# Kernel tuning notes

Measured on AMD Instinct MI355X. Metric: run time of the kernel, lower is better.

The kernel has to match this reference:

```python
import jax, jax.numpy as jnp
import numpy as np

HIDDEN = 1024
HEADS = 16
D_K = HIDDEN // HEADS
B, S = 2, 2048


def setup_inputs() -> dict:
    key = jax.random.key(0)
    ks = jax.random.split(key, 11)
    sc = 1.0 / np.sqrt(HIDDEN)
    return {
        "query": jax.random.normal(ks[0], (B, S, HIDDEN), jnp.float32),
        "key": jax.random.normal(ks[1], (B, S, HIDDEN), jnp.float32),
        "value": jax.random.normal(ks[2], (B, S, HIDDEN), jnp.float32),
        "w_q": jax.random.normal(ks[3], (HIDDEN, HIDDEN), jnp.float32) * sc,
        "b_q": jax.random.normal(ks[4], (HIDDEN,), jnp.float32) * 0.02,
        "w_k": jax.random.normal(ks[5], (HIDDEN, HIDDEN), jnp.float32) * sc,
        "b_k": jax.random.normal(ks[6], (HIDDEN,), jnp.float32) * 0.02,
        "w_v": jax.random.normal(ks[7], (HIDDEN, HIDDEN), jnp.float32) * sc,
        "b_v": jax.random.normal(ks[8], (HIDDEN,), jnp.float32) * 0.02,
        "w_o": jax.random.normal(ks[9], (HIDDEN, HIDDEN), jnp.float32) * sc,
        "b_o": jax.random.normal(ks[10], (HIDDEN,), jnp.float32) * 0.02,
    }


def reference(query, key, value, w_q, b_q, w_k, b_k, w_v, b_v, w_o, b_o):
    b, s, _ = query.shape
    # linear projections (torch Linear: x @ W^T + b)
    q = query @ w_q.T + b_q
    k = key @ w_k.T + b_k
    v = value @ w_v.T + b_v
    # [B, H, S, D]
    q = q.reshape(b, s, HEADS, D_K).transpose(0, 2, 1, 3)
    k = k.reshape(b, s, HEADS, D_K).transpose(0, 2, 1, 3)
    v = v.reshape(b, s, HEADS, D_K).transpose(0, 2, 1, 3)
    scale = jnp.float32(1.0 / np.sqrt(D_K))
    scores = jnp.einsum('bhqd,bhkd->bhqk', q, k) * scale  # [B,H,S,S]
    probs = jax.nn.softmax(scores, axis=-1)
    y = jnp.einsum('bhqk,bhkd->bhqd', probs, v)
    y = y.transpose(0, 2, 1, 3).reshape(b, s, HIDDEN)
    return y @ w_o.T + b_o
```

## Files before the change

### kernel.cpp

```cpp
#include <hip/hip_runtime.h>
#include <hip/hip_bf16.h>
#include <math.h>

#define HIDDEN 1024
#define HEADS 16
#define DK 64
#define BB 2
#define SS 2048
#define MROWS (BB*SS)

typedef __attribute__((ext_vector_type(8))) short short8;
typedef __attribute__((ext_vector_type(4))) float f32x4;
typedef __attribute__((ext_vector_type(16))) float f32x16;
typedef __attribute__((ext_vector_type(4))) unsigned short ushort4_t;

static __device__ __forceinline__ unsigned short f2bf(float f) {
    unsigned int u = __float_as_uint(f);
    u += 0x7fffu + ((u >> 16) & 1u);
    return (unsigned short)(u >> 16);
}
static __device__ __forceinline__ float bf2f(unsigned short s) {
    return __uint_as_float(((unsigned int)s) << 16);
}

static __device__ __forceinline__ unsigned int cvtpk(float lo, float hi) {
    unsigned int r;
    asm volatile("v_cvt_pk_bf16_f32 %0, %1, %2" : "=v"(r) : "v"(lo), "v"(hi));
    return r;
}
static __device__ __forceinline__ void swap32(unsigned int& a, unsigned int& b) {
    asm volatile("v_permlane32_swap_b32 %0, %1" : "+v"(a), "+v"(b));
}
static __device__ __forceinline__ short8 pack_bf16x8(float4 lo, float4 hi) {
    union { unsigned int u[4]; short8 s; } r;
    r.u[0] = cvtpk(lo.x, lo.y);
    r.u[1] = cvtpk(lo.z, lo.w);
    r.u[2] = cvtpk(hi.x, hi.y);
    r.u[3] = cvtpk(hi.z, hi.w);
    return r.s;
}

__global__ __launch_bounds__(256) void cast_w(
    const float* __restrict__ wq, const float* __restrict__ wk, const float* __restrict__ wv,
    unsigned short* __restrict__ Wq, unsigned short* __restrict__ Wk, unsigned short* __restrict__ Wv) {
    int i = blockIdx.x * 256 + threadIdx.x;
    int w = i >> 18, off = i & ((1 << 18) - 1);
    const float* src = (w == 0) ? wq : (w == 1) ? wk : wv;
    unsigned short* dst = (w == 0) ? Wq : (w == 1) ? Wk : Wv;
    float4 f = reinterpret_cast<const float4*>(src)[off];
    ushort4_t o;
    o.x = f2bf(f.x); o.y = f2bf(f.y); o.z = f2bf(f.z); o.w = f2bf(f.w);
    reinterpret_cast<ushort4_t*>(dst)[off] = o;
}

__global__ __launch_bounds__(256, 3) void gemm_qkv(
    const float* __restrict__ Xq, const float* __restrict__ Xk, const float* __restrict__ Xv,
    const unsigned short* __restrict__ Wq, const unsigned short* __restrict__ Wk, const unsigned short* __restrict__ Wv,
    const float* __restrict__ bq, const float* __restrict__ bk, const float* __restrict__ bv,
    unsigned short* __restrict__ Qb, unsigned short* __restrict__ Kb, unsigned short* __restrict__ Vt,
    float scale_q) {
    __shared__ __attribute__((aligned(16))) float Asf[128 * 64];
    __shared__ __attribute__((aligned(16))) unsigned short Bs[128 * 64];
    const int lid = blockIdx.x + 8 * (blockIdx.y + 32 * blockIdx.z);
    const int c = lid & 7, i2 = lid >> 3;
    const int nb = i2 & 7;
    const int band = c * 12 + (i2 >> 3);
    const int yb = band & 31;
    const int z  = band >> 5;
    const float* A           = (z == 0) ? Xq : (z == 1) ? Xk : Xv;
    const unsigned short* Wt = (z == 0) ? Wq : (z == 1) ? Wk : Wv;
    const float* bias = (z == 0) ? bq : (z == 1) ? bk : bv;
    unsigned short* O = (z == 0) ? Qb : (z == 1) ? Kb : Vt;
    const float oscale = (z == 0) ? scale_q : 1.0f;

    const int t    = threadIdx.x;
    const int lane = t & 63;
    const int wave = t >> 6;
    const int m0 = yb * 128;
    const int n0 = nb * 128;

    const int wm = (wave >> 1) * 64;
    const int wn = (wave & 1) * 64;
    const int lr = lane & 15;
    const int g  = lane >> 4;
    const int sr  = lane >> 3;
    const int cs8 = (lane & 7) ^ sr;
    const int ar  = lane >> 4;

    f32x4 acc[4][4];
#pragma unroll
    for (int i = 0; i < 4; i++)
#pragma unroll
        for (int j = 0; j < 4; j++) acc[i][j] = f32x4{0.f, 0.f, 0.f, 0.f};

#define GSTAGE(K0) do {                                                                      \
    _Pragma("unroll")                                                                        \
    for (int jj = 0; jj < 8; jj++) {                                                         \
        int rb = wave * 32 + jj * 4;                                                         \
        int csa = (lane & 15) ^ ((rb + ar) & 15);                                            \
        __builtin_amdgcn_global_load_lds(                                                    \
            (const __attribute__((address_space(1))) unsigned int*)(A + (size_t)(m0 + rb + ar) * HIDDEN + (K0) + csa * 4), \
            (__attribute__((address_space(3))) unsigned int*)&Asf[rb * 64], 16, 0, 0);       \
    }                                                                                        \
    _Pragma("unroll")                                                                        \
    for (int jj = 0; jj < 4; jj++) {                                                         \
        int rb = wave * 32 + jj * 8;                                                         \
        __builtin_amdgcn_global_load_lds(                                                    \
            (const __attribute__((address_space(1))) unsigned int*)(Wt + (size_t)(n0 + rb + sr) * HIDDEN + (K0) + cs8 * 8), \
            (__attribute__((address_space(3))) unsigned int*)&Bs[rb * 64], 16, 0, 0);        \
    }                                                                                        \
} while (0)

    for (int k0 = 0; k0 < HIDDEN; k0 += 64) {
        GSTAGE(k0);
        __syncthreads();
#pragma unroll
        for (int kk = 0; kk < 2; kk++) {
            short8 af[4], bfr[4];
#pragma unroll
            for (int i = 0; i < 4; i++) {
                int row = wm + i * 16 + lr;
                int cg = kk * 8 + g * 2;
                float4 a0 = *reinterpret_cast<const float4*>(&Asf[row * 64 + ((cg     ^ lr) << 2)]);
                float4 a1 = *reinterpret_cast<const float4*>(&Asf[row * 64 + (((cg + 1) ^ lr) << 2)]);
                af[i] = pack_bf16x8(a0, a1);
            }
#pragma unroll
            for (int j = 0; j < 4; j++)
                bfr[j] = *reinterpret_cast<const short8*>(
                    &Bs[(wn + j * 16 + lr) * 64 + (((kk * 4 + g) ^ (lr & 7)) << 3)]);
#pragma unroll
            for (int i = 0; i < 4; i++)
#pragma unroll
                for (int j = 0; j < 4; j++)
                    acc[i][j] = __builtin_amdgcn_mfma_f32_16x16x32_bf16(af[i], bfr[j], acc[i][j], 0, 0, 0);
        }
        __syncthreads();
    }
#undef GSTAGE

#pragma unroll
    for (int i = 0; i < 4; i++) {
        int mrow = m0 + wm + i * 16 + (lane >> 4) * 4;
#pragma unroll
        for (int j = 0; j < 4; j++) {
            int ncol = n0 + wn + j * 16 + lr;
            float bvv = bias[ncol];
            int b_ = mrow >> 11;
            int h_ = ncol >> 6;
            int d_ = ncol & 63;
            if (z != 2) {
#pragma unroll
                for (int r = 0; r < 4; r++) {
                    int s_ = (mrow + r) & 2047;
                    O[(((size_t)(b_ * HEADS + h_)) * SS + s_) * DK + d_] = f2bf((acc[i][j][r] + bvv) * oscale);
                }
            } else {
                int s0 = mrow & 2047;
                ushort4_t pk;
                pk.x = f2bf(acc[i][j][0] + bvv);
                pk.y = f2bf(acc[i][j][1] + bvv);
                pk.z = f2bf(acc[i][j][2] + bvv);
                pk.w = f2bf(acc[i][j][3] + bvv);
                *reinterpret_cast<ushort4_t*>(O + (((size_t)(b_ * HEADS + h_) * DK + d_) * SS + s0)) = pk;
            }
        }
    }
}

__global__ __launch_bounds__(256) void gemm_o(const unsigned short* __restrict__ A,
                                              const float* __restrict__ Wt,
                                              const float* __restrict__ bias,
                                              float* __restrict__ O) {
    __shared__ unsigned short As[128][40];
    __shared__ unsigned short Bs[64][40];
    const int lid = blockIdx.x + 16 * blockIdx.y;
    const int c = lid & 7, i2 = lid >> 3;
    const int nb = i2 & 15;
    const int band = c * 4 + (i2 >> 4);
    const int t    = threadIdx.x;
    const int lane = t & 63;
    const int wave = t >> 6;
    const int m0 = band * 128;
    const int n0 = nb * 64;
    const int row  = t >> 2;
    const int col8 = (t & 3) * 8;

    const int wm = wave * 32;
    const int lr = lane & 15;
    const int lk = (lane >> 4) * 8;

    f32x4 acc[2][4];
#pragma unroll
    for (int i = 0; i < 2; i++)
#pragma unroll
        for (int j = 0; j < 4; j++) acc[i][j] = f32x4{0.f, 0.f, 0.f, 0.f};

    for (int k0 = 0; k0 < HIDDEN; k0 += 32) {
        short8 av0 = *reinterpret_cast<const short8*>(A + (size_t)(m0 + row)      * HIDDEN + k0 + col8);
        short8 av1 = *reinterpret_cast<const short8*>(A + (size_t)(m0 + row + 64) * HIDDEN + k0 + col8);
        const float* w0 = Wt + (size_t)(n0 + row) * HIDDEN + k0 + col8;
        float4 w00 = reinterpret_cast<const float4*>(w0)[0];
        float4 w01 = reinterpret_cast<const float4*>(w0)[1];
        __syncthreads();
        *reinterpret_cast<short8*>(&As[row][col8])      = av0;
        *reinterpret_cast<short8*>(&As[row + 64][col8]) = av1;
        *reinterpret_cast<short8*>(&Bs[row][col8])      = pack_bf16x8(w00, w01);
        __syncthreads();
        short8 af[2], bfr[4];
#pragma unroll
        for (int i = 0; i < 2; i++) af[i]  = *reinterpret_cast<const short8*>(&As[wm + i * 16 + lr][lk]);
#pragma unroll
        for (int j = 0; j < 4; j++) bfr[j] = *reinterpret_cast<const short8*>(&Bs[j * 16 + lr][lk]);
#pragma unroll
        for (int i = 0; i < 2; i++)
#pragma unroll
            for (int j = 0; j < 4; j++)
                acc[i][j] = __builtin_amdgcn_mfma_f32_16x16x32_bf16(af[i], bfr[j], acc[i][j], 0, 0, 0);
    }

#pragma unroll
    for (int i = 0; i < 2; i++) {
        int mrow = m0 + wm + i * 16 + (lane >> 4) * 4;
#pragma unroll
        for (int j = 0; j < 4; j++) {
            int ncol = n0 + j * 16 + lr;
            float bvv = bias[ncol];
#pragma unroll
            for (int r = 0; r < 4; r++)
                O[(size_t)(mrow + r) * HIDDEN + ncol] = acc[i][j][r] + bvv;
        }
    }
}

__global__ __launch_bounds__(256, 4) void attn_kernel(const unsigned short* __restrict__ Qb,
                                                      const unsigned short* __restrict__ Kb,
                                                      const unsigned short* __restrict__ Vt,
                                                      unsigned short* __restrict__ Yb0,
                                                      unsigned short* __restrict__ Yb1,
                                                      float* __restrict__ ml) {
    __shared__ __attribute__((aligned(16))) unsigned short Ksh[2][64 * 64];
    __shared__ __attribute__((aligned(16))) unsigned short Vsh[2][64 * 64];
    __shared__ float Lsh[4][32];

    const int t    = threadIdx.x;
    const int lane = t & 63;
    const int wave = t >> 6;
    const int fid  = blockIdx.x;
    const int c    = fid & 7;
    const int i    = fid >> 3;
    const int qblk = i & 15;
    const int pair = c * 8 + (i >> 4);
    const int bh   = pair >> 1;
    const int kvh  = pair & 1;
    const int b_ = bh >> 4, h_ = bh & 15;
    const int qbase = qblk * 128 + wave * 32;
    const int kvbase = kvh << 10;
    const unsigned short* Qp = Qb + (size_t)bh * SS * DK;
    const unsigned short* Kp = Kb + (size_t)bh * SS * DK;
    const unsigned short* Vp = Vt + (size_t)bh * DK * SS;
    const int lq = lane & 31;
    const int hi = lane >> 5;
    const int sr = lane >> 3;
    const int cs = (lane & 7) ^ sr;

    short8 qf[4];
#pragma unroll
    for (int cc = 0; cc < 4; cc++)
        qf[cc] = *reinterpret_cast<const short8*>(Qp + (size_t)(qbase + lq) * DK + cc * 16 + hi * 8);

    f32x16 acc0, acc1;
#pragma unroll
    for (int r = 0; r < 16; r++) { acc0[r] = 0.f; acc1[r] = 0.f; }
    float li = 0.f;

#define STAGE(BUF, KV0) do {                                                                 \
    __builtin_amdgcn_global_load_lds(                                                        \
        (const __attribute__((address_space(1))) unsigned int*)(Kp + (size_t)((KV0) + wave * 16 + sr) * DK + cs * 8), \
        (__attribute__((address_space(3))) unsigned int*)&Ksh[BUF][(wave * 16) * 64], 16, 0, 0); \
    __builtin_amdgcn_global_load_lds(                                                        \
        (const __attribute__((address_space(1))) unsigned int*)(Kp + (size_t)((KV0) + wave * 16 + 8 + sr) * DK + cs * 8), \
        (__attribute__((address_space(3))) unsigned int*)&Ksh[BUF][(wave * 16 + 8) * 64], 16, 0, 0); \
    __builtin_amdgcn_global_load_lds(                                                        \
        (const __attribute__((address_space(1))) unsigned int*)(Vp + (size_t)(wave * 16 + sr) * SS + (KV0) + cs * 8), \
        (__attribute__((address_space(3))) unsigned int*)&Vsh[BUF][(wave * 16) * 64], 16, 0, 0); \
    __builtin_amdgcn_global_load_lds(                                                        \
        (const __attribute__((address_space(1))) unsigned int*)(Vp + (size_t)(wave * 16 + 8 + sr) * SS + (KV0) + cs * 8), \
        (__attribute__((address_space(3))) unsigned int*)&Vsh[BUF][(wave * 16 + 8) * 64], 16, 0, 0); \
} while (0)

    STAGE(0, kvbase);
    __syncthreads();

    for (int kv0 = kvbase; kv0 < kvbase + 1024; kv0 += 64) {
        const int cur = (kv0 >> 6) & 1;
        if (kv0 + 64 < kvbase + 1024) STAGE(cur ^ 1, kv0 + 64);

        f32x16 sv0, sv1;
#pragma unroll
        for (int r = 0; r < 16; r++) { sv0[r] = 0.f; sv1[r] = 0.f; }
        __builtin_amdgcn_s_setprio(1);
#pragma unroll
        for (int cc = 0; cc < 4; cc++) {
            short8 kf0 = *reinterpret_cast<const short8*>(
                &Ksh[cur][lq * 64 + (((2 * cc + hi) ^ (lq & 7)) << 3)]);
            short8 kf1 = *reinterpret_cast<const short8*>(
                &Ksh[cur][(32 + lq) * 64 + (((2 * cc + hi) ^ (lq & 7)) << 3)]);
            sv0 = __builtin_amdgcn_mfma_f32_32x32x16_bf16(kf0, qf[cc], sv0, 0, 0, 0);
            sv1 = __builtin_amdgcn_mfma_f32_32x32x16_bf16(kf1, qf[cc], sv1, 0, 0, 0);
        }
        __builtin_amdgcn_s_setprio(0);

        float pt[2][16];
        float rs = 0.f;
#pragma unroll
        for (int r = 0; r < 16; r++) {
            pt[0][r] = __builtin_amdgcn_exp2f(sv0[r] - 32.0f);
            pt[1][r] = __builtin_amdgcn_exp2f(sv1[r] - 32.0f);
            rs += pt[0][r] + pt[1][r];
        }
        rs += __shfl_xor(rs, 32);
        li += rs;

        short8 fragP[4];
#pragma unroll
        for (int tt = 0; tt < 2; tt++)
#pragma unroll
            for (int cl = 0; cl < 2; cl++) {
                unsigned int w0 = cvtpk(pt[tt][cl * 8 + 0], pt[tt][cl * 8 + 1]);
                unsigned int w1 = cvtpk(pt[tt][cl * 8 + 2], pt[tt][cl * 8 + 3]);
                unsigned int w2 = cvtpk(pt[tt][cl * 8 + 4], pt[tt][cl * 8 + 5]);
                unsigned int w3 = cvtpk(pt[tt][cl * 8 + 6], pt[tt][cl * 8 + 7]);
                swap32(w0, w2);
                swap32(w1, w3);
                union { unsigned int u[4]; short8 s; } f;
                f.u[0] = w0; f.u[1] = w1; f.u[2] = w2; f.u[3] = w3;
                fragP[tt * 2 + cl] = f.s;
            }

        __builtin_amdgcn_s_setprio(1);
#pragma unroll
        for (int cc = 0; cc < 4; cc++) {
            short8 vf0 = *reinterpret_cast<const short8*>(
                &Vsh[cur][lq * 64 + (((2 * cc + hi) ^ (lq & 7)) << 3)]);
            short8 vf1 = *reinterpret_cast<const short8*>(
                &Vsh[cur][(32 + lq) * 64 + (((2 * cc + hi) ^ (lq & 7)) << 3)]);
            acc0 = __builtin_amdgcn_mfma_f32_32x32x16_bf16(fragP[cc], vf0, acc0, 0, 0, 0);
            acc1 = __builtin_amdgcn_mfma_f32_32x32x16_bf16(fragP[cc], vf1, acc1, 0, 0, 0);
        }
        __builtin_amdgcn_s_setprio(0);
        __syncthreads();
    }
#undef STAGE

    unsigned short* Yp = kvh ? Yb1 : Yb0;
    if (lane < 32) {
        Lsh[wave][lq] = 1.0f / li;
        ml[(((size_t)kvh * 32 + bh) << 11) + qbase + lq] = li;
    }
    __syncthreads();
#pragma unroll
    for (int r = 0; r < 16; r++) {
        int qr = (r & 3) + 8 * (r >> 2) + 4 * hi;
        float inv = Lsh[wave][qr];
        size_t base = ((size_t)b_ * SS + qbase + qr) * HIDDEN + h_ * 64 + lq;
        Yp[base]      = f2bf(acc0[r] * inv);
        Yp[base + 32] = f2bf(acc1[r] * inv);
    }
}

__global__ __launch_bounds__(256) void combine_halves(const unsigned short* __restrict__ Yb0,
                                                      const unsigned short* __restrict__ Yb1,
                                                      const float* __restrict__ ml,
                                                      unsigned short* __restrict__ Yb) {
    int j = blockIdx.x * 256 + threadIdx.x;
    int chunk = j & 127;
    int s = (j >> 7) & 2047;
    int b = j >> 18;
    int h = chunk >> 3;
    int bh = b * 16 + h;
    float l0 = ml[((size_t)bh << 11) + s];
    float l1 = ml[(((size_t)32 + bh) << 11) + s];
    float inv = 1.0f / (l0 + l1);
    float w0 = l0 * inv, w1 = l1 * inv;
    short8 a = reinterpret_cast<const short8*>(Yb0)[j];
    short8 bb = reinterpret_cast<const short8*>(Yb1)[j];
    union { unsigned int u[4]; short8 s8; } o;
#pragma unroll
    for (int k = 0; k < 4; k++) {
        float lo = w0 * bf2f((unsigned short)a[2 * k])     + w1 * bf2f((unsigned short)bb[2 * k]);
        float hi = w0 * bf2f((unsigned short)a[2 * k + 1]) + w1 * bf2f((unsigned short)bb[2 * k + 1]);
        o.u[k] = cvtpk(lo, hi);
    }
    reinterpret_cast<short8*>(Yb)[j] = o.s8;
}

extern "C" void kernel_launch(void* const* d_in, const int* in_sizes, int n_in,
                              void* d_out, int out_size, void* d_ws, size_t ws_size,
                              hipStream_t stream) {
    const float* query = (const float*)d_in[0];
    const float* key_  = (const float*)d_in[1];
    const float* value = (const float*)d_in[2];
    const float* w_q = (const float*)d_in[3];
    const float* b_q = (const float*)d_in[4];
    const float* w_k = (const float*)d_in[5];
    const float* b_k = (const float*)d_in[6];
    const float* w_v = (const float*)d_in[7];
    const float* b_v = (const float*)d_in[8];
    const float* w_o = (const float*)d_in[9];
    const float* b_o = (const float*)d_in[10];

    const size_t SZ_X = (size_t)MROWS * HIDDEN * 2;
    const size_t SZ_W = (size_t)HIDDEN * HIDDEN * 2;
    char* ws = (char*)d_ws;
    unsigned short* Wq = (unsigned short*)(ws);
    unsigned short* Wk = (unsigned short*)(ws + SZ_W);
    unsigned short* Wv = (unsigned short*)(ws + 2 * SZ_W);
    unsigned short* Qb  = (unsigned short*)(ws + 3 * SZ_W);
    unsigned short* Kbf = (unsigned short*)(ws + 3 * SZ_W + SZ_X);
    unsigned short* Vt  = (unsigned short*)(ws + 3 * SZ_W + 2 * SZ_X);
    unsigned short* Yb0 = (unsigned short*)(ws + 3 * SZ_W + 3 * SZ_X);
    unsigned short* Yb1 = (unsigned short*)(ws + 3 * SZ_W + 4 * SZ_X);
    unsigned short* Yb  = (unsigned short*)(ws + 3 * SZ_W + 5 * SZ_X);
    float*          ml  = (float*)(ws + 3 * SZ_W + 6 * SZ_X);

    cast_w<<<3072, 256, 0, stream>>>(w_q, w_k, w_v, Wq, Wk, Wv);

    const float SCALE_Q = 0.125f * 1.4426950408889634f;
    gemm_qkv<<<dim3(8, 32, 3), 256, 0, stream>>>(
        query, key_, value, Wq, Wk, Wv, b_q, b_k, b_v, Qb, Kbf, Vt, SCALE_Q);

    attn_kernel<<<dim3(1024), 256, 0, stream>>>(Qb, Kbf, Vt, Yb0, Yb1, ml);

    combine_halves<<<dim3(2048), 256, 0, stream>>>(Yb0, Yb1, ml, Yb);

    gemm_o<<<dim3(16, 32), 256, 0, stream>>>(Yb, w_o, b_o, (float*)d_out);
}
```

Before: 124.7 us.

## Double-buffer QKV GEMM LDS tiles with K-step 32 and MFMA priority

Splits the QKV projection GEMM's shared-memory tiles into two buffers of K=32 and prefetches the next K slice via global_load_lds while MFMAs run on the current one. This removes one barrier per iteration and hides global load latency behind compute. Swizzle patterns are redone for the narrower rows, and s_setprio raises wave priority around the MFMA block. The cost is twice as many loop iterations with less work between barriers, and possible occupancy or bank-conflict changes.

```diff
diff --git a/kernel.cpp b/kernel.cpp
--- a/kernel.cpp
+++ b/kernel.cpp
@@ -59,8 +59,8 @@
     const float* __restrict__ bq, const float* __restrict__ bk, const float* __restrict__ bv,
     unsigned short* __restrict__ Qb, unsigned short* __restrict__ Kb, unsigned short* __restrict__ Vt,
     float scale_q) {
-    __shared__ __attribute__((aligned(16))) float Asf[128 * 64];
-    __shared__ __attribute__((aligned(16))) unsigned short Bs[128 * 64];
+    __shared__ __attribute__((aligned(16))) float Asf[2][128 * 32];
+    __shared__ __attribute__((aligned(16))) unsigned short Bs[2][128 * 32];
     const int lid = blockIdx.x + 8 * (blockIdx.y + 32 * blockIdx.z);
     const int c = lid & 7, i2 = lid >> 3;
     const int nb = i2 & 7;
@@ -83,9 +83,10 @@
     const int wn = (wave & 1) * 64;
     const int lr = lane & 15;
     const int g  = lane >> 4;
-    const int sr  = lane >> 3;
-    const int cs8 = (lane & 7) ^ sr;
-    const int ar  = lane >> 4;
+    const int sr8 = lane >> 3;
+    const int csA = (lane & 7) ^ sr8;
+    const int sr4 = lane >> 2;
+    const int csB = (lane & 3) ^ ((sr4 >> 1) & 3);
 
     f32x4 acc[4][4];
 #pragma unroll
@@ -93,49 +94,54 @@
 #pragma unroll
         for (int j = 0; j < 4; j++) acc[i][j] = f32x4{0.f, 0.f, 0.f, 0.f};
 
-#define GSTAGE(K0) do {                                                                      \
-    _Pragma("unroll")                                                                        \
-    for (int jj = 0; jj < 8; jj++) {                                                         \
-        int rb = wave * 32 + jj * 4;                                                         \
-        int csa = (lane & 15) ^ ((rb + ar) & 15);                                            \
-        __builtin_amdgcn_global_load_lds(                                                    \
-            (const __attribute__((address_space(1))) unsigned int*)(A + (size_t)(m0 + rb + ar) * HIDDEN + (K0) + csa * 4), \
-            (__attribute__((address_space(3))) unsigned int*)&Asf[rb * 64], 16, 0, 0);       \
-    }                                                                                        \
+#define GSTAGE(BUF, K0) do {                                                                 \
     _Pragma("unroll")                                                                        \
     for (int jj = 0; jj < 4; jj++) {                                                         \
         int rb = wave * 32 + jj * 8;                                                         \
         __builtin_amdgcn_global_load_lds(                                                    \
-            (const __attribute__((address_space(1))) unsigned int*)(Wt + (size_t)(n0 + rb + sr) * HIDDEN + (K0) + cs8 * 8), \
-            (__attribute__((address_space(3))) unsigned int*)&Bs[rb * 64], 16, 0, 0);        \
+            (const __attribute__((address_space(1))) unsigned int*)(A + (size_t)(m0 + rb + sr8) * HIDDEN + (K0) + csA * 4), \
+            (__attribute__((address_space(3))) unsigned int*)&Asf[BUF][rb * 32], 16, 0, 0);  \
+    }                                                                                        \
+    _Pragma("unroll")                                                                        \
+    for (int jj = 0; jj < 2; jj++) {                                                         \
+        int rb = wave * 32 + jj * 16;                                                        \
+        __builtin_amdgcn_global_load_lds(                                                    \
+            (const __attribute__((address_space(1))) unsigned int*)(Wt + (size_t)(n0 + rb + sr4) * HIDDEN + (K0) + csB * 8), \
+            (__attribute__((address_space(3))) unsigned int*)&Bs[BUF][rb * 32], 16, 0, 0);   \
     }                                                                                        \
 } while (0)
 
-    for (int k0 = 0; k0 < HIDDEN; k0 += 64) {
-        GSTAGE(k0);
+    GSTAGE(0, 0);
+    __syncthreads();
+    int cur = 0;
+    for (int k0 = 0; k0 < HIDDEN; k0 += 32) {
+        if (k0 + 32 < HIDDEN) GSTAGE(cur ^ 1, k0 + 32);
+
+        short8 af[4], bfr[4];
+#pragma unroll
+        for (int i = 0; i < 4; i++) {
+            int row = wm + i * 16 + lr;
+            float4 a0 = *reinterpret_cast<const float4*>(
+                &Asf[cur][row * 32 + ((((2 * g)     ^ (lr & 7)) << 2))]);
+            float4 a1 = *reinterpret_cast<const float4*>(
+                &Asf[cur][row * 32 + ((((2 * g + 1) ^ (lr & 7)) << 2))]);
+            af[i] = pack_bf16x8(a0, a1);
+        }
+#pragma unroll
+        for (int j = 0; j < 4; j++)
+            bfr[j] = *reinterpret_cast<const short8*>(
+                &Bs[cur][(wn + j * 16 + lr) * 32 + ((g ^ ((lr >> 1) & 3)) << 3)]);
+
+        __builtin_amdgcn_s_setprio(1);
+#pragma unroll
+        for (int i = 0; i < 4; i++)
+#pragma unroll
+            for (int j = 0; j < 4; j++)
+                acc[i][j] = __builtin_amdgcn_mfma_f32_16x16x32_bf16(af[i], bfr[j], acc[i][j], 0, 0, 0);
+        __builtin_amdgcn_s_setprio(0);
+
         __syncthreads();
-#pragma unroll
-        for (int kk = 0; kk < 2; kk++) {
-            short8 af[4], bfr[4];
-#pragma unroll
-            for (int i = 0; i < 4; i++) {
-                int row = wm + i * 16 + lr;
-                int cg = kk * 8 + g * 2;
-                float4 a0 = *reinterpret_cast<const float4*>(&Asf[row * 64 + ((cg     ^ lr) << 2)]);
-                float4 a1 = *reinterpret_cast<const float4*>(&Asf[row * 64 + (((cg + 1) ^ lr) << 2)]);
-                af[i] = pack_bf16x8(a0, a1);
-            }
-#pragma unroll
-            for (int j = 0; j < 4; j++)
-                bfr[j] = *reinterpret_cast<const short8*>(
-                    &Bs[(wn + j * 16 + lr) * 64 + (((kk * 4 + g) ^ (lr & 7)) << 3)]);
-#pragma unroll
-            for (int i = 0; i < 4; i++)
-#pragma unroll
-                for (int j = 0; j < 4; j++)
-                    acc[i][j] = __builtin_amdgcn_mfma_f32_16x16x32_bf16(af[i], bfr[j], acc[i][j], 0, 0, 0);
-        }
-        __syncthreads();
+        cur ^= 1;
     }
 #undef GSTAGE
 
```

New measurement: 128.1 us. +2.8%, slower.
